# Kernel optimization log

Measured on AMD Instinct MI355X. Metric: run time of the kernel, lower is better.

The kernel has to match this reference:

```python
import jax, jax.numpy as jnp
import numpy as np

EPSILON = 1e-6  # strict '>' inequality adds +epsilon to the correction

B = 2048   # batch
V = 2048   # num variables
C = 512    # num constraints == num anchors (columns 0..C-1)
M = 8      # mask atoms per constraint
H = 16     # attention_hidden_dim


def setup_inputs() -> dict:
    key = jax.random.key(0)
    k = jax.random.split(key, 8)
    preds = jax.random.normal(k[0], (B, V), dtype=jnp.float32)
    ground_truth = jax.random.normal(k[1], (B, V), dtype=jnp.float32)
    # mask variable ids per constraint, drawn from non-anchor columns [C, V)
    mask_ids = jax.random.randint(k[2], (C, M), C, V)
    # per-constraint tiny MLP: Linear(2,H) -> tanh -> Linear(H,1)
    W1 = jax.random.normal(k[3], (C, 2, H), dtype=jnp.float32) * (1.0 / jnp.sqrt(2.0))
    b1 = jax.random.normal(k[4], (C, H), dtype=jnp.float32) * 0.1
    W2 = jax.random.normal(k[5], (C, H), dtype=jnp.float32) * (1.0 / jnp.sqrt(float(H)))
    b2 = jax.random.normal(k[6], (C,), dtype=jnp.float32) * 0.1
    return {"preds": preds, "ground_truth": ground_truth, "mask_ids": mask_ids,
            "W1": W1, "b1": b1, "W2": W2, "b2": b2}


def reference(preds, ground_truth, mask_ids, W1, b1, W2, b2):
    # ground_truth only gates training in the torch module; with our constraint
    # structure (all non-anchor atoms are mask atoms) the GT correction loop is
    # dead code, faithfully reproduced here by not using ground_truth's values.
    del ground_truth
    h_a = preds[:, :C]                                   # [B, C] anchor preds
    h_m = preds[:, mask_ids]                             # [B, C, M] gathered mask preds
    ha_b = jnp.broadcast_to(h_a[:, :, None], h_m.shape)  # [B, C, M]
    feat = jnp.stack([ha_b, h_m], axis=-1)               # [B, C, M, 2]
    hid = jnp.tanh(jnp.einsum('bcmf,cfh->bcmh', feat, W1) + b1[None, :, None, :])
    score = jnp.einsum('bcmh,ch->bcm', hid, W2) + b2[None, :, None]  # [B, C, M]
    attn = jax.nn.softmax(score, axis=-1)                # softmax over mask atoms
    weighted_h_m = jnp.sum(attn * h_m, axis=-1)          # [B, C]
    correction = weighted_h_m + EPSILON                  # strict '>' inequality
    corrected = jnp.maximum(h_a, correction)             # max over {h_A, corrections}
    return preds.at[:, :C].set(corrected)
```

## Files before the change

### kernel.cpp

```cpp
#include <hip/hip_runtime.h>

#define B_ 2048
#define V_ 2048
#define C_ 512
#define M_ 8
#define H_ 16
#define GATH (V_ - C_)
#define ROWS 2

__device__ __forceinline__ float fast_exp2(float x) { return __builtin_amdgcn_exp2f(x); }
__device__ __forceinline__ float fast_rcp(float x)  { return __builtin_amdgcn_rcpf(x); }

#define K_SCALE 2.885390081777927f
#define LOG2E   1.4426950408889634f

__global__ __launch_bounds__(256, 4) void grad_attn_kernel(
    const float* __restrict__ preds,
    const int*   __restrict__ mask_ids,
    const float* __restrict__ W1,
    const float* __restrict__ b1,
    const float* __restrict__ W2,
    float*       __restrict__ out)
{
    __shared__ float smem[ROWS][GATH];

    const int tid = threadIdx.x;
    const int r0  = blockIdx.x * ROWS;

    #pragma unroll
    for (int k = 0; k < ROWS * (GATH / 4) / 256; ++k) {
        int j  = tid + k * 256;
        int r  = j / (GATH / 4);
        int jj = j % (GATH / 4);
        const float4* src = reinterpret_cast<const float4*>(preds + (size_t)(r0 + r) * V_ + C_);
        float4 v = src[jj];
        reinterpret_cast<float4*>(out + (size_t)(r0 + r) * V_ + C_)[jj] = v;
        *reinterpret_cast<float4*>(&smem[r][4 * jj]) = v;
    }
    __syncthreads();

    #pragma unroll
    for (int cc = 0; cc < C_ / 256; ++cc) {
        const int c = tid + cc * 256;

        float w1a[H_], w1b[H_], bb[H_], w2n[H_];
        {
            const float4* W1v = reinterpret_cast<const float4*>(W1 + (size_t)c * 2 * H_);
            const float4* b1v = reinterpret_cast<const float4*>(b1 + (size_t)c * H_);
            const float4* W2v = reinterpret_cast<const float4*>(W2 + (size_t)c * H_);
            #pragma unroll
            for (int i = 0; i < H_ / 4; ++i) {
                float4 a = W1v[i], bk = W1v[H_ / 4 + i], bv = b1v[i], wv = W2v[i];
                w1a[4*i+0] = a.x * K_SCALE;  w1a[4*i+1] = a.y * K_SCALE;
                w1a[4*i+2] = a.z * K_SCALE;  w1a[4*i+3] = a.w * K_SCALE;
                w1b[4*i+0] = bk.x * K_SCALE; w1b[4*i+1] = bk.y * K_SCALE;
                w1b[4*i+2] = bk.z * K_SCALE; w1b[4*i+3] = bk.w * K_SCALE;
                bb[4*i+0]  = bv.x * K_SCALE; bb[4*i+1]  = bv.y * K_SCALE;
                bb[4*i+2]  = bv.z * K_SCALE; bb[4*i+3]  = bv.w * K_SCALE;
                w2n[4*i+0] = -2.0f * wv.x;   w2n[4*i+1] = -2.0f * wv.y;
                w2n[4*i+2] = -2.0f * wv.z;   w2n[4*i+3] = -2.0f * wv.w;
            }
        }

        int midx[M_];
        {
            const int4* mi = reinterpret_cast<const int4*>(mask_ids + (size_t)c * M_);
            int4 a = mi[0], b = mi[1];
            midx[0] = a.x - C_; midx[1] = a.y - C_; midx[2] = a.z - C_; midx[3] = a.w - C_;
            midx[4] = b.x - C_; midx[5] = b.y - C_; midx[6] = b.z - C_; midx[7] = b.w - C_;
        }

        #pragma unroll
        for (int r = 0; r < ROWS; ++r) {
            const float ha = preds[(size_t)(r0 + r) * V_ + c];
            float hm[M_];
            #pragma unroll
            for (int m = 0; m < M_; ++m) hm[m] = smem[r][midx[m]];

            float sc[M_];
            #pragma unroll
            for (int m = 0; m < M_; ++m) sc[m] = 0.0f;

            #pragma unroll
            for (int h = 0; h < H_; ++h) {
                const float pa  = fmaf(ha, w1a[h], bb[h]);
                const float wb  = w1b[h];
                const float w2h = w2n[h];
                #pragma unroll
                for (int m = 0; m < M_; ++m) {
                    float e = fast_exp2(fmaf(hm[m], wb, pa));
                    sc[m] = fmaf(fast_rcp(e + 1.0f), w2h, sc[m]);
                }
            }

            float ex[M_], sum = 0.0f, ws = 0.0f;
            #pragma unroll
            for (int m = 0; m < M_; ++m) {
                ex[m] = fast_exp2(sc[m] * LOG2E);
                sum += ex[m];
            }
            #pragma unroll
            for (int m = 0; m < M_; ++m) ws = fmaf(ex[m], hm[m], ws);
            float corrected = fmaxf(ha, fmaf(ws, fast_rcp(sum), 1e-6f));
            out[(size_t)(r0 + r) * V_ + c] = corrected;
        }
    }
}

extern "C" void kernel_launch(void* const* d_in, const int* in_sizes, int n_in,
                              void* d_out, int out_size, void* d_ws, size_t ws_size,
                              hipStream_t stream) {
    const float* preds    = (const float*)d_in[0];
    const int*   mask_ids = (const int*)d_in[2];
    const float* W1       = (const float*)d_in[3];
    const float* b1       = (const float*)d_in[4];
    const float* W2       = (const float*)d_in[5];
    float* out = (float*)d_out;

    dim3 grid(B_ / ROWS);
    dim3 block(256);
    grad_attn_kernel<<<grid, block, 0, stream>>>(preds, mask_ids, W1, b1, W2, out);
}
```

Before: 38.10 us.

## Map one row per block with one thread per constraint

```diff
diff --git a/kernel.cpp b/kernel.cpp
--- a/kernel.cpp
+++ b/kernel.cpp
@@ -6,7 +6,6 @@
 #define M_ 8
 #define H_ 16
 #define GATH (V_ - C_)
-#define ROWS 2
 
 __device__ __forceinline__ float fast_exp2(float x) { return __builtin_amdgcn_exp2f(x); }
 __device__ __forceinline__ float fast_rcp(float x)  { return __builtin_amdgcn_rcpf(x); }
@@ -14,7 +13,7 @@
 #define K_SCALE 2.885390081777927f
 #define LOG2E   1.4426950408889634f
 
-__global__ __launch_bounds__(256, 4) void grad_attn_kernel(
+__global__ __launch_bounds__(512) void grad_attn_kernel(
     const float* __restrict__ preds,
     const int*   __restrict__ mask_ids,
     const float* __restrict__ W1,
@@ -22,89 +21,80 @@
     const float* __restrict__ W2,
     float*       __restrict__ out)
 {
-    __shared__ float smem[ROWS][GATH];
+    __shared__ float smem[GATH];
 
-    const int tid = threadIdx.x;
-    const int r0  = blockIdx.x * ROWS;
+    const int c   = threadIdx.x;
+    const int row = blockIdx.x;
+    const float* rowp = preds + (size_t)row * V_;
+
+    const float ha = rowp[c];
+
+    float4 cp;
+    if (c < GATH / 4) {
+        cp = reinterpret_cast<const float4*>(rowp + C_)[c];
+        reinterpret_cast<float4*>(out + (size_t)row * V_ + C_)[c] = cp;
+        *reinterpret_cast<float4*>(&smem[4 * c]) = cp;
+    }
+
+    float pa[H_], w1b[H_], w2n[H_];
+    {
+        const float4* W1v = reinterpret_cast<const float4*>(W1 + (size_t)c * 2 * H_);
+        const float4* b1v = reinterpret_cast<const float4*>(b1 + (size_t)c * H_);
+        const float4* W2v = reinterpret_cast<const float4*>(W2 + (size_t)c * H_);
+        #pragma unroll
+        for (int i = 0; i < H_ / 4; ++i) {
+            float4 a = W1v[i], bk = W1v[H_ / 4 + i], bv = b1v[i], wv = W2v[i];
+            pa[4*i+0] = fmaf(ha, a.x, bv.x) * K_SCALE;
+            pa[4*i+1] = fmaf(ha, a.y, bv.y) * K_SCALE;
+            pa[4*i+2] = fmaf(ha, a.z, bv.z) * K_SCALE;
+            pa[4*i+3] = fmaf(ha, a.w, bv.w) * K_SCALE;
+            w1b[4*i+0] = bk.x * K_SCALE; w1b[4*i+1] = bk.y * K_SCALE;
+            w1b[4*i+2] = bk.z * K_SCALE; w1b[4*i+3] = bk.w * K_SCALE;
+            w2n[4*i+0] = -2.0f * wv.x;   w2n[4*i+1] = -2.0f * wv.y;
+            w2n[4*i+2] = -2.0f * wv.z;   w2n[4*i+3] = -2.0f * wv.w;
+        }
+    }
+
+    int midx[M_];
+    {
+        const int4* mi = reinterpret_cast<const int4*>(mask_ids + (size_t)c * M_);
+        int4 a = mi[0], b = mi[1];
+        midx[0] = a.x - C_; midx[1] = a.y - C_; midx[2] = a.z - C_; midx[3] = a.w - C_;
+        midx[4] = b.x - C_; midx[5] = b.y - C_; midx[6] = b.z - C_; midx[7] = b.w - C_;
+    }
+
+    __syncthreads();
+
+    float hm[M_];
+    #pragma unroll
+    for (int m = 0; m < M_; ++m) hm[m] = smem[midx[m]];
+
+    float sc[M_];
+    #pragma unroll
+    for (int m = 0; m < M_; ++m) sc[m] = 0.0f;
 
     #pragma unroll
-    for (int k = 0; k < ROWS * (GATH / 4) / 256; ++k) {
-        int j  = tid + k * 256;
-        int r  = j / (GATH / 4);
-        int jj = j % (GATH / 4);
-        const float4* src = reinterpret_cast<const float4*>(preds + (size_t)(r0 + r) * V_ + C_);
-        float4 v = src[jj];
-        reinterpret_cast<float4*>(out + (size_t)(r0 + r) * V_ + C_)[jj] = v;
-        *reinterpret_cast<float4*>(&smem[r][4 * jj]) = v;
-    }
-    __syncthreads();
-
-    #pragma unroll
-    for (int cc = 0; cc < C_ / 256; ++cc) {
-        const int c = tid + cc * 256;
-
-        float w1a[H_], w1b[H_], bb[H_], w2n[H_];
-        {
-            const float4* W1v = reinterpret_cast<const float4*>(W1 + (size_t)c * 2 * H_);
-            const float4* b1v = reinterpret_cast<const float4*>(b1 + (size_t)c * H_);
-            const float4* W2v = reinterpret_cast<const float4*>(W2 + (size_t)c * H_);
-            #pragma unroll
-            for (int i = 0; i < H_ / 4; ++i) {
-                float4 a = W1v[i], bk = W1v[H_ / 4 + i], bv = b1v[i], wv = W2v[i];
-                w1a[4*i+0] = a.x * K_SCALE;  w1a[4*i+1] = a.y * K_SCALE;
-                w1a[4*i+2] = a.z * K_SCALE;  w1a[4*i+3] = a.w * K_SCALE;
-                w1b[4*i+0] = bk.x * K_SCALE; w1b[4*i+1] = bk.y * K_SCALE;
-                w1b[4*i+2] = bk.z * K_SCALE; w1b[4*i+3] = bk.w * K_SCALE;
-                bb[4*i+0]  = bv.x * K_SCALE; bb[4*i+1]  = bv.y * K_SCALE;
-                bb[4*i+2]  = bv.z * K_SCALE; bb[4*i+3]  = bv.w * K_SCALE;
-                w2n[4*i+0] = -2.0f * wv.x;   w2n[4*i+1] = -2.0f * wv.y;
-                w2n[4*i+2] = -2.0f * wv.z;   w2n[4*i+3] = -2.0f * wv.w;
-            }
-        }
-
-        int midx[M_];
-        {
-            const int4* mi = reinterpret_cast<const int4*>(mask_ids + (size_t)c * M_);
-            int4 a = mi[0], b = mi[1];
-            midx[0] = a.x - C_; midx[1] = a.y - C_; midx[2] = a.z - C_; midx[3] = a.w - C_;
-            midx[4] = b.x - C_; midx[5] = b.y - C_; midx[6] = b.z - C_; midx[7] = b.w - C_;
-        }
-
+    for (int h = 0; h < H_; ++h) {
+        const float pah = pa[h];
+        const float wb  = w1b[h];
+        const float w2h = w2n[h];
         #pragma unroll
-        for (int r = 0; r < ROWS; ++r) {
-            const float ha = preds[(size_t)(r0 + r) * V_ + c];
-            float hm[M_];
-            #pragma unroll
-            for (int m = 0; m < M_; ++m) hm[m] = smem[r][midx[m]];
-
-            float sc[M_];
-            #pragma unroll
-            for (int m = 0; m < M_; ++m) sc[m] = 0.0f;
-
-            #pragma unroll
-            for (int h = 0; h < H_; ++h) {
-                const float pa  = fmaf(ha, w1a[h], bb[h]);
-                const float wb  = w1b[h];
-                const float w2h = w2n[h];
-                #pragma unroll
-                for (int m = 0; m < M_; ++m) {
-                    float e = fast_exp2(fmaf(hm[m], wb, pa));
-                    sc[m] = fmaf(fast_rcp(e + 1.0f), w2h, sc[m]);
-                }
-            }
-
-            float ex[M_], sum = 0.0f, ws = 0.0f;
-            #pragma unroll
-            for (int m = 0; m < M_; ++m) {
-                ex[m] = fast_exp2(sc[m] * LOG2E);
-                sum += ex[m];
-            }
-            #pragma unroll
-            for (int m = 0; m < M_; ++m) ws = fmaf(ex[m], hm[m], ws);
-            float corrected = fmaxf(ha, fmaf(ws, fast_rcp(sum), 1e-6f));
-            out[(size_t)(r0 + r) * V_ + c] = corrected;
+        for (int m = 0; m < M_; ++m) {
+            float e = fast_exp2(fmaf(hm[m], wb, pah));
+            sc[m] = fmaf(fast_rcp(e + 1.0f), w2h, sc[m]);
         }
     }
+
+    float ex[M_], sum = 0.0f, ws = 0.0f;
+    #pragma unroll
+    for (int m = 0; m < M_; ++m) {
+        ex[m] = fast_exp2(sc[m] * LOG2E);
+        sum += ex[m];
+    }
+    #pragma unroll
+    for (int m = 0; m < M_; ++m) ws = fmaf(ex[m], hm[m], ws);
+    float corrected = fmaxf(ha, fmaf(ws, fast_rcp(sum), 1e-6f));
+    out[(size_t)row * V_ + c] = corrected;
 }
 
 extern "C" void kernel_launch(void* const* d_in, const int* in_sizes, int n_in,
@@ -117,7 +107,7 @@
     const float* W2       = (const float*)d_in[5];
     float* out = (float*)d_out;
 
-    dim3 grid(B_ / ROWS);
-    dim3 block(256);
+    dim3 grid(B_);
+    dim3 block(512);
     grad_attn_kernel<<<grid, block, 0, stream>>>(preds, mask_ids, W1, b1, W2, out);
 }
```

Measured after the change: 41.64 us. 9.3% more time.
